# Optimization experiments

Measured on AMD Instinct MI355X. Metric: run time of the kernel, lower is better.

The kernel has to match this reference:

```python
import jax, jax.numpy as jnp
import numpy as np

ALPHA = 0.2  # LeakyReLU negative slope
NEG_INF = -9e15


def setup_inputs() -> dict:
    key = jax.random.key(0)
    k1, k2, k3, k4 = jax.random.split(key, 4)
    B, N, F_in, F_out = 8, 2048, 256, 128
    h = jax.random.normal(k1, (B, N, F_in), dtype=jnp.float32)
    adj = jax.random.randint(k2, (B, N, N), 0, 2, dtype=jnp.int32)
    # xavier_uniform with gain=1.414
    def xavier(k, shape, gain=1.414):
        fan_in, fan_out = shape[0], shape[1]
        limit = gain * np.sqrt(6.0 / (fan_in + fan_out))
        return jax.random.uniform(k, shape, jnp.float32, -limit, limit)
    W = xavier(k3, (F_in, F_out))
    a = xavier(k4, (2 * F_out, 1))
    return {"h": h, "adj": adj, "W": W, "a": a}


def reference(h, adj, W, a):
    # h: [B,N,F_in], adj: [B,N,N], W: [F_in,F_out], a: [2*F_out,1]
    Wh = jnp.einsum('bnf,fe->bne', h, W)  # [B,N,E]
    E = Wh.shape[-1]
    a_src, a_dst = a[:E, 0], a[E:, 0]
    # e[b,i,j] = leakyrelu(Wh[b,i].a_src + Wh[b,j].a_dst)  (additive decomposition
    # of a @ concat(Wh_i, Wh_j) -- same math, no [B,N,N,2E] intermediate)
    s_src = Wh @ a_src  # [B,N]
    s_dst = Wh @ a_dst  # [B,N]
    e = jax.nn.leaky_relu(s_src[:, :, None] + s_dst[:, None, :], negative_slope=ALPHA)
    e = jnp.where(adj > 0, e, NEG_INF)
    attention = jax.nn.softmax(e, axis=2)  # [B,N,N]
    # dropout p=0.0 / eval mode -> identity
    h_prime = jnp.einsum('bij,bje->bie', attention, Wh)
    return jax.nn.elu(h_prime)  # concat=True
```

## Files before the change

### kernel.cpp

```cpp
#include <hip/hip_runtime.h>
#include <hip/hip_bf16.h>

#define GAT_ALPHA 0.2f
#define LOG2E 1.4426950408889634f

typedef float f32x4 __attribute__((ext_vector_type(4)));
typedef int   i32x4 __attribute__((ext_vector_type(4)));
typedef short bf16x8 __attribute__((ext_vector_type(8)));

static constexpr int Nn  = 2048;
static constexpr int FIN = 256;
static constexpr int FO  = 128;

static __device__ __forceinline__ unsigned short f2bf(float x) {
    __hip_bfloat16 h = __float2bfloat16(x);
    return __builtin_bit_cast(unsigned short, h);
}
static __device__ __forceinline__ float bf2f(unsigned short u) {
    unsigned int v = ((unsigned int)u) << 16;
    return __builtin_bit_cast(float, v);
}

__global__ __launch_bounds__(256) void gat_prep(
        const float* __restrict__ W, const float* __restrict__ a,
        float* __restrict__ wa, unsigned int* __restrict__ md_key)
{
    __shared__ float pr[32][8];
    __shared__ float pd[32][8];
    const int t = threadIdx.x;
    const int kl = t >> 3, seg = t & 7;
    const int k = blockIdx.x * 32 + kl;
    float ps = 0.f, pv = 0.f;
    const float* wr = W + (size_t)k * FO + seg * 16;
    #pragma unroll
    for (int f = 0; f < 16; f += 4) {
        f32x4 wv = *(const f32x4*)(wr + f);
        f32x4 as = *(const f32x4*)(a + seg * 16 + f);
        f32x4 ad = *(const f32x4*)(a + FO + seg * 16 + f);
        ps += wv[0]*as[0] + wv[1]*as[1] + wv[2]*as[2] + wv[3]*as[3];
        pv += wv[0]*ad[0] + wv[1]*ad[1] + wv[2]*ad[2] + wv[3]*ad[3];
    }
    pr[kl][seg] = ps; pd[kl][seg] = pv;
    __syncthreads();
    if (t < 32) {
        float s = 0.f, d = 0.f;
        #pragma unroll
        for (int j = 0; j < 8; ++j) { s += pr[t][j]; d += pd[t][j]; }
        wa[blockIdx.x * 32 + t]       = s;
        wa[256 + blockIdx.x * 32 + t] = d;
    }
    if (blockIdx.x == 0 && t < 8) md_key[t] = 0u;
}

__global__ __launch_bounds__(256) void gat_wh(
        const float* __restrict__ h, const float* __restrict__ W,
        const float* __restrict__ wa, unsigned short* __restrict__ WhT,
        float* __restrict__ s_src, float* __restrict__ s_dst,
        unsigned int* __restrict__ md_key)
{
    __shared__ unsigned short WT[FO][264];
    __shared__ float wal[512];
    __shared__ float sred[64][4][2];
    __shared__ float red64[64];
    const int t  = threadIdx.x;
    const int b  = blockIdx.x & 7;
    const int n0 = (blockIdx.x >> 3) << 6;

    if (t < 128) *(f32x4*)&wal[t * 4] = *(const f32x4*)&wa[t * 4];
    #pragma unroll
    for (int c = 0; c < 32; ++c) {
        int flat = c * 1024 + t * 4;
        int k = flat >> 7, f = flat & 127;
        f32x4 wv = *(const f32x4*)&W[flat];
        WT[f + 0][k] = f2bf(wv[0]);
        WT[f + 1][k] = f2bf(wv[1]);
        WT[f + 2][k] = f2bf(wv[2]);
        WT[f + 3][k] = f2bf(wv[3]);
    }
    __syncthreads();

    {
        const int row = t >> 2, seg = t & 3;
        const float* hp  = h + ((size_t)(b * Nn + n0 + row)) * FIN + seg * 64;
        const float* was = &wal[seg * 64];
        const float* wad = &wal[256 + seg * 64];
        float ps = 0.f, pv = 0.f;
        #pragma unroll
        for (int j = 0; j < 64; j += 4) {
            f32x4 hv = *(const f32x4*)(hp + j);
            f32x4 sv = *(const f32x4*)(was + j);
            f32x4 dv = *(const f32x4*)(wad + j);
            ps += hv[0]*sv[0] + hv[1]*sv[1] + hv[2]*sv[2] + hv[3]*sv[3];
            pv += hv[0]*dv[0] + hv[1]*dv[1] + hv[2]*dv[2] + hv[3]*dv[3];
        }
        sred[row][seg][0] = ps;
        sred[row][seg][1] = pv;
    }
    __syncthreads();
    if (t < 64) {
        float s = sred[t][0][0] + sred[t][1][0] + sred[t][2][0] + sred[t][3][0];
        float d = sred[t][0][1] + sred[t][1][1] + sred[t][2][1] + sred[t][3][1];
        s_src[b * Nn + n0 + t] = s;
        s_dst[b * Nn + n0 + t] = d;
        red64[t] = d;
    }
    __syncthreads();
    if (t < 16) red64[t] = fmaxf(fmaxf(red64[t], red64[t + 16]),
                                 fmaxf(red64[t + 32], red64[t + 48]));
    __syncthreads();
    if (t == 0) {
        float m = red64[0];
        #pragma unroll
        for (int j = 1; j < 16; ++j) m = fmaxf(m, red64[j]);
        unsigned int bits = __builtin_bit_cast(unsigned int, m);
        unsigned int key  = (bits & 0x80000000u) ? ~bits : (bits | 0x80000000u);
        atomicMax(md_key + b, key);
    }

    const int w = t >> 6, lane = t & 63, n16 = lane & 15, quad = lane >> 4;
    const float* ha = h + ((size_t)(b * Nn + n0 + w * 16 + n16)) * FIN + quad * 8;
    f32x4 acc[8] = {};
    #pragma unroll
    for (int ks = 0; ks < 8; ++ks) {
        f32x4 h0 = *(const f32x4*)(ha + ks * 32);
        f32x4 h1 = *(const f32x4*)(ha + ks * 32 + 4);
        bf16x8 af;
        af[0] = (short)f2bf(h0[0]); af[1] = (short)f2bf(h0[1]);
        af[2] = (short)f2bf(h0[2]); af[3] = (short)f2bf(h0[3]);
        af[4] = (short)f2bf(h1[0]); af[5] = (short)f2bf(h1[1]);
        af[6] = (short)f2bf(h1[2]); af[7] = (short)f2bf(h1[3]);
        #pragma unroll
        for (int nt = 0; nt < 8; ++nt) {
            bf16x8 bfr = *(const bf16x8*)&WT[nt * 16 + n16][ks * 32 + quad * 8];
            acc[nt] = __builtin_amdgcn_mfma_f32_16x16x32_bf16(af, bfr, acc[nt], 0, 0, 0);
        }
    }
    #pragma unroll
    for (int nt = 0; nt < 8; ++nt) {
        ushort4 pk;
        pk.x = f2bf(acc[nt][0]); pk.y = f2bf(acc[nt][1]);
        pk.z = f2bf(acc[nt][2]); pk.w = f2bf(acc[nt][3]);
        *(ushort4*)&WhT[((size_t)(b * FO + nt * 16 + n16)) * Nn + n0 + w * 16 + quad * 4] = pk;
    }
}

__global__ __launch_bounds__(256, 3) void gat_attn(
        const int* __restrict__ adj, const unsigned short* __restrict__ WhT,
        const float* __restrict__ s_src, const float* __restrict__ s_dst,
        const unsigned int* __restrict__ md_key, float* __restrict__ out)
{
    constexpr int WS = 136;
    constexpr int PS = 136;
    constexpr int AS = 132;
    __shared__ __align__(16) unsigned short whs[128 * WS];
    __shared__ __align__(16) unsigned short psT[32 * PS];
    __shared__ float l_red[32];
    float* accbuf = (float*)whs;

    const int t = threadIdx.x, w = t >> 6, lane = t & 63;
    const int n16 = lane & 15, quad = lane >> 4;
    const int b  = blockIdx.x & 7;
    const int i0 = (blockIdx.x >> 3) << 5;
    const int r  = t >> 3;
    const int jg = t & 7;

    if (t < 32) l_red[t] = 0.f;

    const unsigned int key = md_key[b];
    const unsigned int mb  = (key & 0x80000000u) ? (key ^ 0x80000000u) : ~key;
    const float mdb = __builtin_bit_cast(float, mb);
    const float ssr = s_src[b * Nn + i0 + r];
    const float tm  = ssr + mdb;
    const float mi  = fmaxf(tm, GAT_ALPHA * tm) * LOG2E;
    const float ssL = ssr * LOG2E;

    const int* arow = adj + ((size_t)(b * Nn + i0 + r)) * Nn;
    const float* dB = s_dst + b * Nn;
    const unsigned short* wrow = WhT + ((size_t)(b * FO + (w << 5))) * Nn;
    const int fsub = lane >> 4;
    const int jc16 = lane & 15;

    f32x4 acc[2][8] = {};
    float ls = 0.f;

    i32x4 pa[4];
    #pragma unroll
    for (int k = 0; k < 4; ++k) pa[k] = *(const i32x4*)(arow + (jg << 2) + (k << 5));

    for (int s = 0; s < 16; ++s) {
        const int j0 = s << 7;
        bf16x8 wreg[8];
        #pragma unroll
        for (int i = 0; i < 8; ++i)
            wreg[i] = *(const bf16x8*)(wrow + (size_t)((i << 2) + fsub) * Nn + j0 + (jc16 << 3));
        float e16[16];
        #pragma unroll
        for (int k = 0; k < 4; ++k) {
            f32x4 dv = *(const f32x4*)(dB + j0 + (jg << 2) + (k << 5));
            #pragma unroll
            for (int j = 0; j < 4; ++j) {
                float u  = __builtin_fmaf(dv[j], LOG2E, ssL);
                float lr = fmaxf(u, GAT_ALPHA * u);
                float e  = __builtin_amdgcn_exp2f(lr - mi);
                e16[k * 4 + j] = (pa[k][j] > 0) ? e : 0.f;
            }
        }
        const int jn = (s < 15) ? (j0 + 128) : 0;
        #pragma unroll
        for (int k = 0; k < 4; ++k) pa[k] = *(const i32x4*)(arow + jn + (jg << 2) + (k << 5));
        #pragma unroll
        for (int k = 0; k < 4; ++k) {
            unsigned short u0 = f2bf(e16[k*4+0]), u1 = f2bf(e16[k*4+1]);
            unsigned short u2 = f2bf(e16[k*4+2]), u3 = f2bf(e16[k*4+3]);
            ls += bf2f(u0) + bf2f(u1) + bf2f(u2) + bf2f(u3);
            ushort4 pk; pk.x = u0; pk.y = u1; pk.z = u2; pk.w = u3;
            *(ushort4*)&psT[r * PS + (jg << 2) + (k << 5)] = pk;
        }
        #pragma unroll
        for (int i = 0; i < 8; ++i)
            *(bf16x8*)&whs[((w << 5) + (i << 2) + fsub) * WS + (jc16 << 3)] = wreg[i];
        __syncthreads();
        bf16x8 bfr[8];
        #pragma unroll
        for (int nt = 0; nt < 8; ++nt)
            bfr[nt] = *(const bf16x8*)&whs[((nt << 4) + n16) * WS + (w << 5) + (quad << 3)];
        #pragma unroll
        for (int ig = 0; ig < 2; ++ig) {
            bf16x8 af = *(const bf16x8*)&psT[((ig << 4) + n16) * PS + (w << 5) + (quad << 3)];
            #pragma unroll
            for (int nt = 0; nt < 8; ++nt)
                acc[ig][nt] = __builtin_amdgcn_mfma_f32_16x16x32_bf16(af, bfr[nt], acc[ig][nt], 0, 0, 0);
        }
        __syncthreads();
    }

    atomicAdd(&l_red[r], ls);
    if (w < 2) {
        #pragma unroll
        for (int ig = 0; ig < 2; ++ig)
            #pragma unroll
            for (int nt = 0; nt < 8; ++nt)
                #pragma unroll
                for (int rr = 0; rr < 4; ++rr)
                    accbuf[(size_t)w * 32 * AS + (ig * 16 + quad * 4 + rr) * AS + nt * 16 + n16] = acc[ig][nt][rr];
    }
    __syncthreads();
    if (w >= 2) {
        #pragma unroll
        for (int ig = 0; ig < 2; ++ig)
            #pragma unroll
            for (int nt = 0; nt < 8; ++nt)
                #pragma unroll
                for (int rr = 0; rr < 4; ++rr)
                    accbuf[(size_t)(w - 2) * 32 * AS + (ig * 16 + quad * 4 + rr) * AS + nt * 16 + n16] += acc[ig][nt][rr];
    }
    __syncthreads();
    float* ob = out + ((size_t)(b * Nn + i0)) * FO;
    #pragma unroll
    for (int c = 0; c < 4; ++c) {
        int flat = c * 1024 + t * 4;
        int m = flat >> 7, f = flat & 127;
        f32x4 v0 = *(const f32x4*)&accbuf[(size_t)m * AS + f];
        f32x4 v1 = *(const f32x4*)&accbuf[(size_t)32 * AS + m * AS + f];
        float l = l_red[m];
        f32x4 o;
        #pragma unroll
        for (int j = 0; j < 4; ++j) {
            float x = (v0[j] + v1[j]) / l;
            o[j] = x > 0.f ? x : expm1f(x);
        }
        *(f32x4*)&ob[(size_t)m * FO + f] = o;
    }
}

extern "C" void kernel_launch(void* const* d_in, const int* in_sizes, int n_in,
                              void* d_out, int out_size, void* d_ws, size_t ws_size,
                              hipStream_t stream)
{
    const float* h   = (const float*)d_in[0];
    const int*   adj = (const int*)d_in[1];
    const float* W   = (const float*)d_in[2];
    const float* a   = (const float*)d_in[3];
    float* out = (float*)d_out;

    char* ws = (char*)d_ws;
    unsigned short* WhT = (unsigned short*)ws;
    float* s_src        = (float*)(ws + 4194304);
    float* s_dst        = (float*)(ws + 4259840);
    float* wa           = (float*)(ws + 4325376);
    unsigned int* md_key= (unsigned int*)(ws + 4327424);

    hipLaunchKernelGGL(gat_prep, dim3(8),   dim3(256), 0, stream, W, a, wa, md_key);
    hipLaunchKernelGGL(gat_wh,   dim3(256), dim3(256), 0, stream, h, W, wa, WhT, s_src, s_dst, md_key);
    hipLaunchKernelGGL(gat_attn, dim3(512), dim3(256), 0, stream, adj, WhT, s_src, s_dst, md_key, out);
}
```

Measured before the change: 236.3 us.

## Compute attention weights directly in MFMA register layout, drop LDS staging

The attention kernel now has each lane compute its exp weights straight into the MFMA A-operand layout and load WhT fragments from global memory directly into B-operand registers. This removes the per-tile LDS writes/reads and both __syncthreads per iteration. Row-sum reduction moves to wave shuffles followed by a few atomics. Launch bounds drop from 3 to 2 blocks per SM, and global loads are now less coalesced (16-byte strided per lane across rows), which may raise memory traffic cost.

```diff
diff --git a/kernel.cpp b/kernel.cpp
--- a/kernel.cpp
+++ b/kernel.cpp
@@ -144,97 +144,114 @@
     }
 }
 
-__global__ __launch_bounds__(256, 3) void gat_attn(
+__global__ __launch_bounds__(256, 2) void gat_attn(
         const int* __restrict__ adj, const unsigned short* __restrict__ WhT,
         const float* __restrict__ s_src, const float* __restrict__ s_dst,
         const unsigned int* __restrict__ md_key, float* __restrict__ out)
 {
-    constexpr int WS = 136;
-    constexpr int PS = 136;
     constexpr int AS = 132;
-    __shared__ __align__(16) unsigned short whs[128 * WS];
-    __shared__ __align__(16) unsigned short psT[32 * PS];
+    __shared__ __align__(16) float accbuf[2 * 32 * AS];
     __shared__ float l_red[32];
-    float* accbuf = (float*)whs;
 
     const int t = threadIdx.x, w = t >> 6, lane = t & 63;
     const int n16 = lane & 15, quad = lane >> 4;
     const int b  = blockIdx.x & 7;
     const int i0 = (blockIdx.x >> 3) << 5;
-    const int r  = t >> 3;
-    const int jg = t & 7;
 
     if (t < 32) l_red[t] = 0.f;
+    __syncthreads();
 
     const unsigned int key = md_key[b];
     const unsigned int mb  = (key & 0x80000000u) ? (key ^ 0x80000000u) : ~key;
     const float mdb = __builtin_bit_cast(float, mb);
-    const float ssr = s_src[b * Nn + i0 + r];
-    const float tm  = ssr + mdb;
-    const float mi  = fmaxf(tm, GAT_ALPHA * tm) * LOG2E;
-    const float ssL = ssr * LOG2E;
-
-    const int* arow = adj + ((size_t)(b * Nn + i0 + r)) * Nn;
-    const float* dB = s_dst + b * Nn;
-    const unsigned short* wrow = WhT + ((size_t)(b * FO + (w << 5))) * Nn;
-    const int fsub = lane >> 4;
-    const int jc16 = lane & 15;
+
+    const float ssr0 = s_src[b * Nn + i0 + n16];
+    const float ssr1 = s_src[b * Nn + i0 + 16 + n16];
+    const float tm0 = ssr0 + mdb, tm1 = ssr1 + mdb;
+    const float mi0 = fmaxf(tm0, GAT_ALPHA * tm0) * LOG2E;
+    const float mi1 = fmaxf(tm1, GAT_ALPHA * tm1) * LOG2E;
+    const float sL0 = ssr0 * LOG2E, sL1 = ssr1 * LOG2E;
+
+    const int jw = (w << 5) + (quad << 3);
+    const int* ap0 = adj + ((size_t)(b * Nn + i0 + n16)) * Nn + jw;
+    const int* ap1 = ap0 + (size_t)16 * Nn;
+    const float* dptr = s_dst + b * Nn + jw;
+    const unsigned short* wptr = WhT + ((size_t)(b * FO + n16)) * Nn + jw;
 
     f32x4 acc[2][8] = {};
-    float ls = 0.f;
+    float ls0 = 0.f, ls1 = 0.f;
 
     i32x4 pa[4];
-    #pragma unroll
-    for (int k = 0; k < 4; ++k) pa[k] = *(const i32x4*)(arow + (jg << 2) + (k << 5));
+    pa[0] = *(const i32x4*)(ap0);
+    pa[1] = *(const i32x4*)(ap0 + 4);
+    pa[2] = *(const i32x4*)(ap1);
+    pa[3] = *(const i32x4*)(ap1 + 4);
 
     for (int s = 0; s < 16; ++s) {
         const int j0 = s << 7;
-        bf16x8 wreg[8];
-        #pragma unroll
-        for (int i = 0; i < 8; ++i)
-            wreg[i] = *(const bf16x8*)(wrow + (size_t)((i << 2) + fsub) * Nn + j0 + (jc16 << 3));
-        float e16[16];
-        #pragma unroll
-        for (int k = 0; k < 4; ++k) {
-            f32x4 dv = *(const f32x4*)(dB + j0 + (jg << 2) + (k << 5));
-            #pragma unroll
-            for (int j = 0; j < 4; ++j) {
-                float u  = __builtin_fmaf(dv[j], LOG2E, ssL);
+        bf16x8 bfr[8];
+        #pragma unroll
+        for (int nt = 0; nt < 8; ++nt)
+            bfr[nt] = *(const bf16x8*)(wptr + (size_t)(nt << 4) * Nn + j0);
+        f32x4 d0 = *(const f32x4*)(dptr + j0);
+        f32x4 d1 = *(const f32x4*)(dptr + j0 + 4);
+        const int jn = (s < 15) ? (j0 + 128) : 0;
+        i32x4 na0 = *(const i32x4*)(ap0 + jn);
+        i32x4 na1 = *(const i32x4*)(ap0 + jn + 4);
+        i32x4 na2 = *(const i32x4*)(ap1 + jn);
+        i32x4 na3 = *(const i32x4*)(ap1 + jn + 4);
+
+        bf16x8 af0, af1;
+        #pragma unroll
+        for (int j = 0; j < 4; ++j) {
+            {
+                float u  = __builtin_fmaf(d0[j], LOG2E, sL0);
                 float lr = fmaxf(u, GAT_ALPHA * u);
-                float e  = __builtin_amdgcn_exp2f(lr - mi);
-                e16[k * 4 + j] = (pa[k][j] > 0) ? e : 0.f;
+                float e  = __builtin_amdgcn_exp2f(lr - mi0);
+                e = (pa[0][j] > 0) ? e : 0.f;
+                unsigned short us = f2bf(e);
+                ls0 += bf2f(us); af0[j] = (short)us;
             }
-        }
-        const int jn = (s < 15) ? (j0 + 128) : 0;
-        #pragma unroll
-        for (int k = 0; k < 4; ++k) pa[k] = *(const i32x4*)(arow + jn + (jg << 2) + (k << 5));
-        #pragma unroll
-        for (int k = 0; k < 4; ++k) {
-            unsigned short u0 = f2bf(e16[k*4+0]), u1 = f2bf(e16[k*4+1]);
-            unsigned short u2 = f2bf(e16[k*4+2]), u3 = f2bf(e16[k*4+3]);
-            ls += bf2f(u0) + bf2f(u1) + bf2f(u2) + bf2f(u3);
-            ushort4 pk; pk.x = u0; pk.y = u1; pk.z = u2; pk.w = u3;
-            *(ushort4*)&psT[r * PS + (jg << 2) + (k << 5)] = pk;
-        }
-        #pragma unroll
-        for (int i = 0; i < 8; ++i)
-            *(bf16x8*)&whs[((w << 5) + (i << 2) + fsub) * WS + (jc16 << 3)] = wreg[i];
-        __syncthreads();
-        bf16x8 bfr[8];
-        #pragma unroll
-        for (int nt = 0; nt < 8; ++nt)
-            bfr[nt] = *(const bf16x8*)&whs[((nt << 4) + n16) * WS + (w << 5) + (quad << 3)];
-        #pragma unroll
-        for (int ig = 0; ig < 2; ++ig) {
-            bf16x8 af = *(const bf16x8*)&psT[((ig << 4) + n16) * PS + (w << 5) + (quad << 3)];
-            #pragma unroll
-            for (int nt = 0; nt < 8; ++nt)
-                acc[ig][nt] = __builtin_amdgcn_mfma_f32_16x16x32_bf16(af, bfr[nt], acc[ig][nt], 0, 0, 0);
-        }
-        __syncthreads();
-    }
-
-    atomicAdd(&l_red[r], ls);
+            {
+                float u  = __builtin_fmaf(d1[j], LOG2E, sL0);
+                float lr = fmaxf(u, GAT_ALPHA * u);
+                float e  = __builtin_amdgcn_exp2f(lr - mi0);
+                e = (pa[1][j] > 0) ? e : 0.f;
+                unsigned short us = f2bf(e);
+                ls0 += bf2f(us); af0[4 + j] = (short)us;
+            }
+            {
+                float u  = __builtin_fmaf(d0[j], LOG2E, sL1);
+                float lr = fmaxf(u, GAT_ALPHA * u);
+                float e  = __builtin_amdgcn_exp2f(lr - mi1);
+                e = (pa[2][j] > 0) ? e : 0.f;
+                unsigned short us = f2bf(e);
+                ls1 += bf2f(us); af1[j] = (short)us;
+            }
+            {
+                float u  = __builtin_fmaf(d1[j], LOG2E, sL1);
+                float lr = fmaxf(u, GAT_ALPHA * u);
+                float e  = __builtin_amdgcn_exp2f(lr - mi1);
+                e = (pa[3][j] > 0) ? e : 0.f;
+                unsigned short us = f2bf(e);
+                ls1 += bf2f(us); af1[4 + j] = (short)us;
+            }
+        }
+        #pragma unroll
+        for (int nt = 0; nt < 8; ++nt) {
+            acc[0][nt] = __builtin_amdgcn_mfma_f32_16x16x32_bf16(af0, bfr[nt], acc[0][nt], 0, 0, 0);
+            acc[1][nt] = __builtin_amdgcn_mfma_f32_16x16x32_bf16(af1, bfr[nt], acc[1][nt], 0, 0, 0);
+        }
+        pa[0] = na0; pa[1] = na1; pa[2] = na2; pa[3] = na3;
+    }
+
+    ls0 += __shfl_xor(ls0, 16); ls0 += __shfl_xor(ls0, 32);
+    ls1 += __shfl_xor(ls1, 16); ls1 += __shfl_xor(ls1, 32);
+    if (quad == 0) {
+        atomicAdd(&l_red[n16], ls0);
+        atomicAdd(&l_red[16 + n16], ls1);
+    }
+
     if (w < 2) {
         #pragma unroll
         for (int ig = 0; ig < 2; ++ig)
```

New measurement: 253.1 us. +7.1%, slower.

## Pre-pack Wh into MFMA fragment layout and drop LDS staging in attention

Applied to the files above, without the earlier changes.

The Wh projection kernel now writes Wh in a pre-swizzled layout that matches the MFMA B-operand fragment, so the attention kernel loads B fragments straight from global memory. Each lane computes its own attention probabilities directly in A-fragment layout, which removes the LDS staging and both barriers per tile. The row tile shrinks from 32 to 16 rows, doubling the grid and raising the occupancy hint to 4. In exchange, the Wh fragments are re-read from global/L2 by twice as many blocks, and each wave issues half as many MFMAs per loaded B fragment.

```diff
diff --git a/kernel.cpp b/kernel.cpp
--- a/kernel.cpp
+++ b/kernel.cpp
@@ -54,7 +54,7 @@
 
 __global__ __launch_bounds__(256) void gat_wh(
         const float* __restrict__ h, const float* __restrict__ W,
-        const float* __restrict__ wa, unsigned short* __restrict__ WhT,
+        const float* __restrict__ wa, unsigned short* __restrict__ Wp,
         float* __restrict__ s_src, float* __restrict__ s_dst,
         unsigned int* __restrict__ md_key)
 {
@@ -135,133 +135,123 @@
             acc[nt] = __builtin_amdgcn_mfma_f32_16x16x32_bf16(af, bfr, acc[nt], 0, 0, 0);
         }
     }
-    #pragma unroll
-    for (int nt = 0; nt < 8; ++nt) {
-        ushort4 pk;
-        pk.x = f2bf(acc[nt][0]); pk.y = f2bf(acc[nt][1]);
-        pk.z = f2bf(acc[nt][2]); pk.w = f2bf(acc[nt][3]);
-        *(ushort4*)&WhT[((size_t)(b * FO + nt * 16 + n16)) * Nn + n0 + w * 16 + quad * 4] = pk;
-    }
-}
-
-__global__ __launch_bounds__(256, 3) void gat_attn(
-        const int* __restrict__ adj, const unsigned short* __restrict__ WhT,
+    {
+        const int v      = (n0 >> 5) + (w >> 1);
+        const int quad_p = ((w & 1) << 1) + (quad >> 1);
+        const int eoff   = (quad & 1) << 2;
+        #pragma unroll
+        for (int nt = 0; nt < 8; ++nt) {
+            ushort4 pk;
+            pk.x = f2bf(acc[nt][0]); pk.y = f2bf(acc[nt][1]);
+            pk.z = f2bf(acc[nt][2]); pk.w = f2bf(acc[nt][3]);
+            size_t idx = ((((size_t)(b << 6) + v) * 8 + nt) * 64 + quad_p * 16 + n16) * 8 + eoff;
+            *(ushort4*)&Wp[idx] = pk;
+        }
+    }
+}
+
+__global__ __launch_bounds__(256, 4) void gat_attn(
+        const int* __restrict__ adj, const unsigned short* __restrict__ Wp,
         const float* __restrict__ s_src, const float* __restrict__ s_dst,
         const unsigned int* __restrict__ md_key, float* __restrict__ out)
 {
-    constexpr int WS = 136;
-    constexpr int PS = 136;
     constexpr int AS = 132;
-    __shared__ __align__(16) unsigned short whs[128 * WS];
-    __shared__ __align__(16) unsigned short psT[32 * PS];
-    __shared__ float l_red[32];
-    float* accbuf = (float*)whs;
+    __shared__ __align__(16) float accbuf[2 * 16 * AS];
+    __shared__ float l_red[16];
 
     const int t = threadIdx.x, w = t >> 6, lane = t & 63;
     const int n16 = lane & 15, quad = lane >> 4;
     const int b  = blockIdx.x & 7;
-    const int i0 = (blockIdx.x >> 3) << 5;
-    const int r  = t >> 3;
-    const int jg = t & 7;
-
-    if (t < 32) l_red[t] = 0.f;
+    const int i0 = (blockIdx.x >> 3) << 4;
+
+    if (t < 16) l_red[t] = 0.f;
+    __syncthreads();
 
     const unsigned int key = md_key[b];
     const unsigned int mb  = (key & 0x80000000u) ? (key ^ 0x80000000u) : ~key;
     const float mdb = __builtin_bit_cast(float, mb);
-    const float ssr = s_src[b * Nn + i0 + r];
+
+    const float ssr = s_src[b * Nn + i0 + n16];
     const float tm  = ssr + mdb;
     const float mi  = fmaxf(tm, GAT_ALPHA * tm) * LOG2E;
-    const float ssL = ssr * LOG2E;
-
-    const int* arow = adj + ((size_t)(b * Nn + i0 + r)) * Nn;
-    const float* dB = s_dst + b * Nn;
-    const unsigned short* wrow = WhT + ((size_t)(b * FO + (w << 5))) * Nn;
-    const int fsub = lane >> 4;
-    const int jc16 = lane & 15;
-
-    f32x4 acc[2][8] = {};
+    const float sL  = ssr * LOG2E;
+
+    const int jw = (w << 5) + (quad << 3);
+    const int* ap    = adj + ((size_t)(b * Nn + i0 + n16)) * Nn + jw;
+    const float* dptr = s_dst + b * Nn + jw;
+    const unsigned short* wp = Wp + ((size_t)b << 18) + ((size_t)w << 12) + (lane << 3);
+
+    f32x4 acc[8] = {};
     float ls = 0.f;
 
-    i32x4 pa[4];
-    #pragma unroll
-    for (int k = 0; k < 4; ++k) pa[k] = *(const i32x4*)(arow + (jg << 2) + (k << 5));
+    i32x4 pa0 = *(const i32x4*)(ap);
+    i32x4 pa1 = *(const i32x4*)(ap + 4);
 
     for (int s = 0; s < 16; ++s) {
         const int j0 = s << 7;
-        bf16x8 wreg[8];
-        #pragma unroll
-        for (int i = 0; i < 8; ++i)
-            wreg[i] = *(const bf16x8*)(wrow + (size_t)((i << 2) + fsub) * Nn + j0 + (jc16 << 3));
-        float e16[16];
-        #pragma unroll
-        for (int k = 0; k < 4; ++k) {
-            f32x4 dv = *(const f32x4*)(dB + j0 + (jg << 2) + (k << 5));
+        const unsigned short* wts = wp + (s << 14);
+        bf16x8 bfr[8];
+        #pragma unroll
+        for (int nt = 0; nt < 8; ++nt)
+            bfr[nt] = *(const bf16x8*)(wts + (nt << 9));
+        f32x4 d0 = *(const f32x4*)(dptr + j0);
+        f32x4 d1 = *(const f32x4*)(dptr + j0 + 4);
+        const int jn = (s < 15) ? (j0 + 128) : 0;
+        i32x4 na0 = *(const i32x4*)(ap + jn);
+        i32x4 na1 = *(const i32x4*)(ap + jn + 4);
+
+        bf16x8 af;
+        #pragma unroll
+        for (int j = 0; j < 4; ++j) {
+            float u  = __builtin_fmaf(d0[j], LOG2E, sL);
+            float lr = fmaxf(u, GAT_ALPHA * u);
+            float e  = __builtin_amdgcn_exp2f(lr - mi);
+            e = (pa0[j] > 0) ? e : 0.f;
+            unsigned short us = f2bf(e);
+            ls += bf2f(us); af[j] = (short)us;
+        }
+        #pragma unroll
+        for (int j = 0; j < 4; ++j) {
+            float u  = __builtin_fmaf(d1[j], LOG2E, sL);
+            float lr = fmaxf(u, GAT_ALPHA * u);
+            float e  = __builtin_amdgcn_exp2f(lr - mi);
+            e = (pa1[j] > 0) ? e : 0.f;
+            unsigned short us = f2bf(e);
+            ls += bf2f(us); af[4 + j] = (short)us;
+        }
+        #pragma unroll
+        for (int nt = 0; nt < 8; ++nt)
+            acc[nt] = __builtin_amdgcn_mfma_f32_16x16x32_bf16(af, bfr[nt], acc[nt], 0, 0, 0);
+        pa0 = na0; pa1 = na1;
+    }
+
+    ls += __shfl_xor(ls, 16); ls += __shfl_xor(ls, 32);
+    if (quad == 0) atomicAdd(&l_red[n16], ls);
+
+    float* slot = accbuf + (size_t)(w & 1) * 16 * AS;
+    if (w < 2) {
+        #pragma unroll
+        for (int nt = 0; nt < 8; ++nt)
             #pragma unroll
-            for (int j = 0; j < 4; ++j) {
-                float u  = __builtin_fmaf(dv[j], LOG2E, ssL);
-                float lr = fmaxf(u, GAT_ALPHA * u);
-                float e  = __builtin_amdgcn_exp2f(lr - mi);
-                e16[k * 4 + j] = (pa[k][j] > 0) ? e : 0.f;
-            }
-        }
-        const int jn = (s < 15) ? (j0 + 128) : 0;
-        #pragma unroll
-        for (int k = 0; k < 4; ++k) pa[k] = *(const i32x4*)(arow + jn + (jg << 2) + (k << 5));
-        #pragma unroll
-        for (int k = 0; k < 4; ++k) {
-            unsigned short u0 = f2bf(e16[k*4+0]), u1 = f2bf(e16[k*4+1]);
-            unsigned short u2 = f2bf(e16[k*4+2]), u3 = f2bf(e16[k*4+3]);
-            ls += bf2f(u0) + bf2f(u1) + bf2f(u2) + bf2f(u3);
-            ushort4 pk; pk.x = u0; pk.y = u1; pk.z = u2; pk.w = u3;
-            *(ushort4*)&psT[r * PS + (jg << 2) + (k << 5)] = pk;
-        }
-        #pragma unroll
-        for (int i = 0; i < 8; ++i)
-            *(bf16x8*)&whs[((w << 5) + (i << 2) + fsub) * WS + (jc16 << 3)] = wreg[i];
-        __syncthreads();
-        bf16x8 bfr[8];
-        #pragma unroll
-        for (int nt = 0; nt < 8; ++nt)
-            bfr[nt] = *(const bf16x8*)&whs[((nt << 4) + n16) * WS + (w << 5) + (quad << 3)];
-        #pragma unroll
-        for (int ig = 0; ig < 2; ++ig) {
-            bf16x8 af = *(const bf16x8*)&psT[((ig << 4) + n16) * PS + (w << 5) + (quad << 3)];
+            for (int rr = 0; rr < 4; ++rr)
+                slot[(quad * 4 + rr) * AS + nt * 16 + n16] = acc[nt][rr];
+    }
+    __syncthreads();
+    if (w >= 2) {
+        #pragma unroll
+        for (int nt = 0; nt < 8; ++nt)
             #pragma unroll
-            for (int nt = 0; nt < 8; ++nt)
-                acc[ig][nt] = __builtin_amdgcn_mfma_f32_16x16x32_bf16(af, bfr[nt], acc[ig][nt], 0, 0, 0);
-        }
-        __syncthreads();
-    }
-
-    atomicAdd(&l_red[r], ls);
-    if (w < 2) {
-        #pragma unroll
-        for (int ig = 0; ig < 2; ++ig)
-            #pragma unroll
-            for (int nt = 0; nt < 8; ++nt)
-                #pragma unroll
-                for (int rr = 0; rr < 4; ++rr)
-                    accbuf[(size_t)w * 32 * AS + (ig * 16 + quad * 4 + rr) * AS + nt * 16 + n16] = acc[ig][nt][rr];
-    }
-    __syncthreads();
-    if (w >= 2) {
-        #pragma unroll
-        for (int ig = 0; ig < 2; ++ig)
-            #pragma unroll
-            for (int nt = 0; nt < 8; ++nt)
-                #pragma unroll
-                for (int rr = 0; rr < 4; ++rr)
-                    accbuf[(size_t)(w - 2) * 32 * AS + (ig * 16 + quad * 4 + rr) * AS + nt * 16 + n16] += acc[ig][nt][rr];
+            for (int rr = 0; rr < 4; ++rr)
+                slot[(quad * 4 + rr) * AS + nt * 16 + n16] += acc[nt][rr];
     }
     __syncthreads();
     float* ob = out + ((size_t)(b * Nn + i0)) * FO;
     #pragma unroll
-    for (int c = 0; c < 4; ++c) {
+    for (int c = 0; c < 2; ++c) {
         int flat = c * 1024 + t * 4;
         int m = flat >> 7, f = flat & 127;
         f32x4 v0 = *(const f32x4*)&accbuf[(size_t)m * AS + f];
-        f32x4 v1 = *(const f32x4*)&accbuf[(size_t)32 * AS + m * AS + f];
+        f32x4 v1 = *(const f32x4*)&accbuf[(size_t)16 * AS + m * AS + f];
         float l = l_red[m];
         f32x4 o;
         #pragma unroll
@@ -284,13 +274,13 @@
     float* out = (float*)d_out;
 
     char* ws = (char*)d_ws;
-    unsigned short* WhT = (unsigned short*)ws;
+    unsigned short* Wp  = (unsigned short*)ws;
     float* s_src        = (float*)(ws + 4194304);
     float* s_dst        = (float*)(ws + 4259840);
     float* wa           = (float*)(ws + 4325376);
     unsigned int* md_key= (unsigned int*)(ws + 4327424);
 
-    hipLaunchKernelGGL(gat_prep, dim3(8),   dim3(256), 0, stream, W, a, wa, md_key);
-    hipLaunchKernelGGL(gat_wh,   dim3(256), dim3(256), 0, stream, h, W, wa, WhT, s_src, s_dst, md_key);
-    hipLaunchKernelGGL(gat_attn, dim3(512), dim3(256), 0, stream, adj, WhT, s_src, s_dst, md_key, out);
-}
+    hipLaunchKernelGGL(gat_prep, dim3(8),    dim3(256), 0, stream, W, a, wa, md_key);
+    hipLaunchKernelGGL(gat_wh,   dim3(256),  dim3(256), 0, stream, h, W, wa, Wp, s_src, s_dst, md_key);
+    hipLaunchKernelGGL(gat_attn, dim3(1024), dim3(256), 0, stream, adj, Wp, s_src, s_dst, md_key, out);
+}
```

Result: slower. 257.5 us (+9.0%).
